# Performance work log

Hardware: AMD Instinct MI355X
Metric: run time of the kernel (lower is better)

The kernel has to match this reference:

```python
import jax, jax.numpy as jnp
import numpy as np

K = 3
KK = K * K
G = 8  # num_heads / offset groups
PAD = K // 2


def conv2d(x, w, b):
    # NCHW conv, stride 1, same padding
    y = jax.lax.conv_general_dilated(
        x, w, window_strides=(1, 1), padding=[(PAD, PAD), (PAD, PAD)],
        dimension_numbers=("NCHW", "OIHW", "NCHW"))
    return y + b[None, :, None, None]


def bilinear_sample(img, py, px):
    # img: [Cg, H, W]; py/px: [KK, H, W] fractional sampling locations
    # zero-padding bilinear (torchvision deform_conv2d semantics)
    Cg, H, W = img.shape
    flat = img.reshape(Cg, H * W)

    y0 = jnp.floor(py)
    x0 = jnp.floor(px)
    wy1 = py - y0
    wx1 = px - x0
    wy0 = 1.0 - wy1
    wx0 = 1.0 - wx1
    y0i = y0.astype(jnp.int32)
    x0i = x0.astype(jnp.int32)

    def gather(iy, ix):
        valid = (iy >= 0) & (iy < H) & (ix >= 0) & (ix < W)
        idx = jnp.clip(iy, 0, H - 1) * W + jnp.clip(ix, 0, W - 1)
        v = jnp.take(flat, idx.reshape(-1), axis=1).reshape(Cg, KK, H, W)
        return v * valid[None].astype(img.dtype)

    return (gather(y0i, x0i) * (wy0 * wx0)[None]
            + gather(y0i, x0i + 1) * (wy0 * wx1)[None]
            + gather(y0i + 1, x0i) * (wy1 * wx0)[None]
            + gather(y0i + 1, x0i + 1) * (wy1 * wx1)[None])


def setup_inputs() -> dict:
    key = jax.random.key(0)
    ks = jax.random.split(key, 8)
    B, C, H, W = 8, 256, 64, 64
    O = 256
    x = jax.random.normal(ks[0], (B, C, H, W), jnp.float32)
    w_off = jax.random.normal(ks[1], (2 * KK * G, C, K, K), jnp.float32) * 0.01
    b_off = jax.random.normal(ks[2], (2 * KK * G,), jnp.float32) * 0.01
    w_attn = jax.random.normal(ks[3], (KK * G, C, K, K), jnp.float32) * 0.01
    b_attn = jax.random.normal(ks[4], (KK * G,), jnp.float32) * 0.01
    w_out = jax.random.normal(ks[5], (O, C, K, K), jnp.float32) * 0.02
    b_out = jax.random.normal(ks[6], (O,), jnp.float32) * 0.01
    return {"x": x, "w_off": w_off, "b_off": b_off,
            "w_attn": w_attn, "b_attn": b_attn,
            "w_out": w_out, "b_out": b_out}


def reference(x, w_off, b_off, w_attn, b_attn, w_out, b_out):
    B, C, H, W = x.shape
    O = w_out.shape[0]
    Cg = C // G

    # learned offsets: [B, G, KK, 2(dy,dx), H, W]
    off = conv2d(x, w_off, b_off).reshape(B, G, KK, 2, H, W)
    # modulation mask with softmax over the KK kernel taps (per head)
    attn = conv2d(x, w_attn, b_attn).reshape(B, G, KK, H, W)
    attn = jax.nn.softmax(attn, axis=2)

    # base sampling grid for each kernel tap (stride=1, dilation=1)
    ki = (jnp.arange(KK) // K).astype(x.dtype)  # kernel row
    kj = (jnp.arange(KK) % K).astype(x.dtype)   # kernel col
    base_y = jnp.arange(H, dtype=x.dtype)[None, :, None] - PAD + ki[:, None, None]  # [KK,H,1]
    base_x = jnp.arange(W, dtype=x.dtype)[None, None, :] - PAD + kj[:, None, None]  # [KK,1,W]
    py = base_y + off[:, :, :, 0]  # [B,G,KK,H,W]
    px = base_x + off[:, :, :, 1]

    xg = x.reshape(B, G, Cg, H, W)
    # vmap bilinear gather over batch and offset groups -> [B,G,Cg,KK,H,W]
    samp = jax.vmap(jax.vmap(bilinear_sample))(xg, py, px)

    # modulated deformable conv: mask-weight the samples, contract with weights
    wt = w_out.reshape(O, G, Cg, KK)
    out = jnp.einsum("bgnkhw,bgkhw,ognk->bohw", samp, attn, wt)
    return out + b_out[None, :, None, None]
```

## Files before the change

### kernel.cpp

```cpp
#include <hip/hip_runtime.h>

#define BN   8
#define CC   256
#define HH   64
#define WW   64
#define GG   8
#define CG   32
#define KKK  9
#define OO   256
#define HW   (HH*WW)
#define NPAD 256
#define NOUT 216

#define XH   68
#define XROW (XH*256)
#define XB   (XH*XH*256)

typedef __attribute__((ext_vector_type(8))) _Float16 half8;
typedef __attribute__((ext_vector_type(4))) float f32x4;

union U4H8 { uint4 u; half8 h; };

#define LGKM0_BARRIER() do { \
    asm volatile("s_waitcnt lgkmcnt(0)" ::: "memory"); \
    __builtin_amdgcn_s_barrier(); \
    __builtin_amdgcn_sched_barrier(0); \
} while (0)

__global__ void repack_w(const float* __restrict__ w_out, _Float16* __restrict__ wt3) {
    int idx = blockIdx.x * 256 + threadIdx.x;
    if (idx >= GG * KKK * CG * OO) return;
    int e    = idx & 7;
    int lane = (idx >> 3) & 63;
    int ot   = (idx >> 9) & 15;
    int s    = idx >> 13;
    int kk = s % 9;
    int g  = s / 9;
    int oc = ot * 16 + (lane & 15);
    int cg = (lane >> 4) * 8 + e;
    wt3[idx] = (_Float16)w_out[oc * 2304 + (g * 32 + cg) * 9 + kk];
}

__global__ void repack_conv(const float* __restrict__ w_off, const float* __restrict__ b_off,
                            const float* __restrict__ w_attn, const float* __restrict__ b_attn,
                            _Float16* __restrict__ wt_conv, float* __restrict__ bias_c) {
    int idx = blockIdx.x * 256 + threadIdx.x;
    if (idx >= 9 * NPAD * 256) return;
    int e    = idx & 7;
    int lane = (idx >> 3) & 63;
    int ot   = (idx >> 9) & 15;
    int gs   = idx >> 13;
    int tap = gs >> 3;
    int ch  = (gs & 7) * 32 + (lane >> 4) * 8 + e;
    int n   = ot * 16 + (lane & 15);
    float v = 0.f;
    if (n < 144)      v = w_off[(n * 256 + ch) * 9 + tap];
    else if (n < 216) v = w_attn[((n - 144) * 256 + ch) * 9 + tap];
    wt_conv[idx] = (_Float16)v;
    if (idx < 224) {
        float bv = 0.f;
        if (idx < 144)      bv = b_off[idx];
        else if (idx < 216) bv = b_attn[idx - 144];
        bias_c[idx] = bv;
    }
}

__global__ __launch_bounds__(256) void repack_x(const float* __restrict__ x,
                                                _Float16* __restrict__ x_h) {
    __shared__ _Float16 T[64][264];
    const int bid = blockIdx.x;
    const int b = bid & 7, h = bid >> 3;
    const int t = threadIdx.x;
    const float* src = x + (((long)(b * 256 + t)) << 12) + h * 64;
    #pragma unroll
    for (int i = 0; i < 16; ++i) {
        float4 f = ((const float4*)src)[i];
        T[i * 4 + 0][t] = (_Float16)f.x;
        T[i * 4 + 1][t] = (_Float16)f.y;
        T[i * 4 + 2][t] = (_Float16)f.z;
        T[i * 4 + 3][t] = (_Float16)f.w;
    }
    __syncthreads();
    _Float16* dst = x_h + ((long)(b * XH + h + 2) * XH + 2) * 256;
    #pragma unroll
    for (int it = 0; it < 8; ++it) {
        int idx = it * 256 + t;
        int px = idx >> 5, ch = idx & 31;
        uint4 v = *(const uint4*)&T[px][ch * 8];
        *(uint4*)(dst + px * 256 + ch * 8) = v;
    }
}

__global__ __launch_bounds__(512, 4) void conv_mfma(
    const _Float16* __restrict__ x_h, const _Float16* __restrict__ wt_conv,
    const float* __restrict__ bias_c, float* __restrict__ conv_buf) {
    __shared__ alignas(16) char smem[36864];
    _Float16 (*Ald)[2][64][40] = (_Float16 (*)[2][64][40])smem;
    float* red = (float*)smem;

    const int bid = blockIdx.x;
    const int b = bid & 7, h = bid >> 3;
    const int t = threadIdx.x;
    const int lane = t & 63;
    const int wv = t >> 6;
    const int group = wv >> 2;
    const int wg = wv & 3;
    const int tl = t & 255;
    const int px = tl >> 2, cq = tl & 3;
    const int gs0 = group * 36;

    f32x4 acc[4][4];
    #pragma unroll
    for (int i = 0; i < 4; ++i)
        #pragma unroll
        for (int j = 0; j < 4; ++j) acc[i][j] = (f32x4){0.f, 0.f, 0.f, 0.f};

    const _Float16* xb = x_h + (long)b * XB + cq * 8;
    const _Float16* wB = wt_conv + (long)(wg * 256 + lane) * 8;

    uint4 aR;
    uint4 bq0, bq1, bq2, bq3;

    {
        int tap = gs0 >> 3, cc = gs0 & 7;
        int y = h + tap / 3 + 1, xc = px + tap % 3 + 1;
        uint4 a0 = *(const uint4*)(xb + ((long)(y * XH + xc)) * 256 + cc * 32);
        *(uint4*)&Ald[group][0][px][cq * 8] = a0;
    }
    {
        int gsn = gs0 + 1;
        int tap = gsn >> 3, cc = gsn & 7;
        int y = h + tap / 3 + 1, xc = px + tap % 3 + 1;
        aR = *(const uint4*)(xb + ((long)(y * XH + xc)) * 256 + cc * 32);
    }
    {
        const _Float16* wsB = wB + (long)gs0 * 8192;
        bq0 = *(const uint4*)(wsB);
        bq1 = *(const uint4*)(wsB + 512);
        bq2 = *(const uint4*)(wsB + 1024);
        bq3 = *(const uint4*)(wsB + 1536);
    }
    LGKM0_BARRIER();

    for (int s = 0; s < 36; ++s) {
        const int gs = gs0 + s;
        if (s < 35) {
            *(uint4*)&Ald[group][(s + 1) & 1][px][cq * 8] = aR;
        }
        if (s < 34) {
            int gsn = gs + 2;
            int tap = gsn >> 3, cc = gsn & 7;
            int y = h + tap / 3 + 1, xc = px + tap % 3 + 1;
            aR = *(const uint4*)(xb + ((long)(y * XH + xc)) * 256 + cc * 32);
        }
        {
            const int k0 = (lane >> 4) * 8;
            U4H8 b0, b1, b2, b3; b0.u = bq0; b1.u = bq1; b2.u = bq2; b3.u = bq3;
            #pragma unroll
            for (int mi = 0; mi < 4; ++mi) {
                half8 a = *(const half8*)&Ald[group][s & 1][mi * 16 + (lane & 15)][k0];
                acc[mi][0] = __builtin_amdgcn_mfma_f32_16x16x32_f16(a, b0.h, acc[mi][0], 0, 0, 0);
                acc[mi][1] = __builtin_amdgcn_mfma_f32_16x16x32_f16(a, b1.h, acc[mi][1], 0, 0, 0);
                acc[mi][2] = __builtin_amdgcn_mfma_f32_16x16x32_f16(a, b2.h, acc[mi][2], 0, 0, 0);
                acc[mi][3] = __builtin_amdgcn_mfma_f32_16x16x32_f16(a, b3.h, acc[mi][3], 0, 0, 0);
            }
        }
        if (s < 35) {
            const _Float16* wsB = wB + (long)(gs + 1) * 8192;
            bq0 = *(const uint4*)(wsB);
            bq1 = *(const uint4*)(wsB + 512);
            bq2 = *(const uint4*)(wsB + 1024);
            bq3 = *(const uint4*)(wsB + 1536);
        }
        LGKM0_BARRIER();
    }

    #pragma unroll
    for (int r = 0; r < 2; ++r) {
        __syncthreads();
        if (group == 1) {
            #pragma unroll
            for (int m2 = 0; m2 < 2; ++m2)
                #pragma unroll
                for (int j = 0; j < 4; ++j)
                    *(f32x4*)&red[tl * 36 + m2 * 16 + j * 4] = acc[r * 2 + m2][j];
        }
        __syncthreads();
        if (group == 0) {
            #pragma unroll
            for (int m2 = 0; m2 < 2; ++m2)
                #pragma unroll
                for (int j = 0; j < 4; ++j) {
                    f32x4 v = *(const f32x4*)&red[tl * 36 + m2 * 16 + j * 4];
                    acc[r * 2 + m2][j] += v;
                }
        }
    }

    if (group == 0) {
        const int colb = (lane >> 4) * 4;
        #pragma unroll
        for (int mi = 0; mi < 4; ++mi) {
            int px0 = mi * 16 + colb;
            #pragma unroll
            for (int j = 0; j < 4; ++j) {
                int oc = wg * 64 + j * 16 + (lane & 15);
                if (oc < NOUT) {
                    float bb = bias_c[oc];
                    float4 v = make_float4(acc[mi][j][0] + bb, acc[mi][j][1] + bb,
                                           acc[mi][j][2] + bb, acc[mi][j][3] + bb);
                    *(float4*)&conv_buf[((long)b * NOUT + oc) * HW + h * WW + px0] = v;
                }
            }
        }
    }
}

__device__ __forceinline__ void calc_coords(int h, int px, int ki, int kj,
    float dy, float dx, int& i00,
    float& u00, float& u01, float& u10, float& u11) {
    float py  = (float)(h - 1 + ki) + dy;
    float pxf = (float)(px - 1 + kj) + dx;
    float y0f = floorf(py), x0f = floorf(pxf);
    float wy1 = py - y0f, wx1 = pxf - x0f;
    float wy0 = 1.f - wy1, wx0 = 1.f - wx1;
    int y0 = min(max((int)y0f, -2), 64);
    int x0 = min(max((int)x0f, -2), 64);
    u00 = wy0 * wx0; u01 = wy0 * wx1;
    u10 = wy1 * wx0; u11 = wy1 * wx1;
    i00 = (y0 + 2) * XH + (x0 + 2);
}

__global__ __launch_bounds__(512, 4) void sample_gemm_mfma(
    const _Float16* __restrict__ x_h, const float* __restrict__ conv_buf,
    const _Float16* __restrict__ wt3,
    const float* __restrict__ b_out, float* __restrict__ out) {
    __shared__ alignas(16) char smem[38912];
    _Float16 (*Ald)[2][64][40] = (_Float16 (*)[2][64][40])smem;
    float* attnL = (float*)(smem + 20480);
    float* red = (float*)smem;

    const int bid = blockIdx.x;
    const int b = bid & 7, h = bid >> 3;
    const int t = threadIdx.x;
    const int lane = t & 63;
    const int wv = t >> 6;
    const int group = wv >> 2;
    const int wg = wv & 3;
    const int tl = t & 255;
    const int px = tl >> 2, cq = tl & 3;
    const int gs0 = group * 36;

    f32x4 acc[4][4];
    #pragma unroll
    for (int i = 0; i < 4; ++i)
        #pragma unroll
        for (int j = 0; j < 4; ++j) acc[i][j] = (f32x4){0.f, 0.f, 0.f, 0.f};

    const float* cbase = conv_buf + (long)b * NOUT * HW + h * WW;
    const _Float16* xbase = x_h + (long)b * XB + cq * 8;
    const _Float16* wB3 = wt3 + (long)(wg * 256 + lane) * 8;

    {
        int ppx = t & 63, g = t >> 6;
        const float* ap = cbase + (long)(144 + g * 9) * HW + ppx;
        float v[9];
        float m = -1e30f;
        #pragma unroll
        for (int k = 0; k < 9; ++k) { v[k] = ap[k * HW]; m = fmaxf(m, v[k]); }
        float ssum = 0.f;
        #pragma unroll
        for (int k = 0; k < 9; ++k) { v[k] = __expf(v[k] - m); ssum += v[k]; }
        float inv = 1.f / ssum;
        #pragma unroll
        for (int k = 0; k < 9; ++k) attnL[(g * 9 + k) * 64 + ppx] = v[k] * inv;
    }
    float dy0 = cbase[(2 * gs0) * HW + px], dx0 = cbase[(2 * gs0 + 1) * HW + px];
    __syncthreads();

    uint4 q00, q01, q10, q11;
    float u00, u01, u10, u11;
    float dyN, dxN;
    uint4 bq0, bq1, bq2, bq3;
    {
        int i00;
        float v00, v01, v10, v11;
        calc_coords(h, px, 0, 0, dy0, dx0, i00, v00, v01, v10, v11);
        const _Float16* xg = xbase + (group * 4) * 32 + (long)i00 * 256;
        uint4 a00 = *(const uint4*)(xg);
        uint4 a01 = *(const uint4*)(xg + 256);
        uint4 a10 = *(const uint4*)(xg + XROW);
        uint4 a11 = *(const uint4*)(xg + XROW + 256);
        float av = attnL[gs0 * 64 + px];
        U4H8 h00, h01, h10, h11;
        h00.u = a00; h01.u = a01; h10.u = a10; h11.u = a11;
        half8 rr = h00.h * (_Float16)v00 + h01.h * (_Float16)v01
                 + h10.h * (_Float16)v10 + h11.h * (_Float16)v11;
        rr = rr * (_Float16)av;
        *(half8*)&Ald[group][0][px][cq * 8] = rr;
    }
    {
        float dy1 = cbase[(2 * (gs0 + 1)) * HW + px];
        float dx1 = cbase[(2 * (gs0 + 1) + 1) * HW + px];
        int i00;
        calc_coords(h, px, 0, 1, dy1, dx1, i00, u00, u01, u10, u11);
        const _Float16* xg = xbase + (group * 4) * 32 + (long)i00 * 256;
        q00 = *(const uint4*)(xg);
        q01 = *(const uint4*)(xg + 256);
        q10 = *(const uint4*)(xg + XROW);
        q11 = *(const uint4*)(xg + XROW + 256);
        dyN = cbase[(2 * (gs0 + 2)) * HW + px];
        dxN = cbase[(2 * (gs0 + 2) + 1) * HW + px];
    }
    {
        const _Float16* wsB = wB3 + (long)gs0 * 8192;
        bq0 = *(const uint4*)(wsB);
        bq1 = *(const uint4*)(wsB + 512);
        bq2 = *(const uint4*)(wsB + 1024);
        bq3 = *(const uint4*)(wsB + 1536);
    }
    LGKM0_BARRIER();

    for (int s = 0; s < 36; ++s) {
        const int gs = gs0 + s;
        if (s < 35) {
            float av = attnL[(gs + 1) * 64 + px];
            U4H8 a00, a01, a10, a11;
            a00.u = q00; a01.u = q01; a10.u = q10; a11.u = q11;
            half8 rr = a00.h * (_Float16)u00 + a01.h * (_Float16)u01
                     + a10.h * (_Float16)u10 + a11.h * (_Float16)u11;
            rr = rr * (_Float16)av;
            *(half8*)&Ald[group][(s + 1) & 1][px][cq * 8] = rr;
        }
        if (s < 34) {
            int sn = s + 2;
            int g = group * 4 + sn / 9, kk = sn % 9;
            int i00;
            calc_coords(h, px, kk / 3, kk % 3, dyN, dxN, i00, u00, u01, u10, u11);
            const _Float16* xg = xbase + g * 32 + (long)i00 * 256;
            q00 = *(const uint4*)(xg);
            q01 = *(const uint4*)(xg + 256);
            q10 = *(const uint4*)(xg + XROW);
            q11 = *(const uint4*)(xg + XROW + 256);
            int s3 = min(s + 3, 35);
            dyN = cbase[(2 * (gs0 + s3)) * HW + px];
            dxN = cbase[(2 * (gs0 + s3) + 1) * HW + px];
        }
        {
            const int k0 = (lane >> 4) * 8;
            U4H8 b0, b1, b2, b3; b0.u = bq0; b1.u = bq1; b2.u = bq2; b3.u = bq3;
            #pragma unroll
            for (int mi = 0; mi < 4; ++mi) {
                half8 a = *(const half8*)&Ald[group][s & 1][mi * 16 + (lane & 15)][k0];
                acc[mi][0] = __builtin_amdgcn_mfma_f32_16x16x32_f16(a, b0.h, acc[mi][0], 0, 0, 0);
                acc[mi][1] = __builtin_amdgcn_mfma_f32_16x16x32_f16(a, b1.h, acc[mi][1], 0, 0, 0);
                acc[mi][2] = __builtin_amdgcn_mfma_f32_16x16x32_f16(a, b2.h, acc[mi][2], 0, 0, 0);
                acc[mi][3] = __builtin_amdgcn_mfma_f32_16x16x32_f16(a, b3.h, acc[mi][3], 0, 0, 0);
            }
        }
        if (s < 35) {
            const _Float16* wsB = wB3 + (long)(gs + 1) * 8192;
            bq0 = *(const uint4*)(wsB);
            bq1 = *(const uint4*)(wsB + 512);
            bq2 = *(const uint4*)(wsB + 1024);
            bq3 = *(const uint4*)(wsB + 1536);
        }
        LGKM0_BARRIER();
    }

    #pragma unroll
    for (int r = 0; r < 2; ++r) {
        __syncthreads();
        if (group == 1) {
            #pragma unroll
            for (int m2 = 0; m2 < 2; ++m2)
                #pragma unroll
                for (int j = 0; j < 4; ++j)
                    *(f32x4*)&red[tl * 36 + m2 * 16 + j * 4] = acc[r * 2 + m2][j];
        }
        __syncthreads();
        if (group == 0) {
            #pragma unroll
            for (int m2 = 0; m2 < 2; ++m2)
                #pragma unroll
                for (int j = 0; j < 4; ++j) {
                    f32x4 v = *(const f32x4*)&red[tl * 36 + m2 * 16 + j * 4];
                    acc[r * 2 + m2][j] += v;
                }
        }
    }

    if (group == 0) {
        const int colb = (lane >> 4) * 4;
        #pragma unroll
        for (int mi = 0; mi < 4; ++mi) {
            int px0 = mi * 16 + colb;
            #pragma unroll
            for (int j = 0; j < 4; ++j) {
                int oc = wg * 64 + j * 16 + (lane & 15);
                float bb = b_out[oc];
                float4 v = make_float4(acc[mi][j][0] + bb, acc[mi][j][1] + bb,
                                       acc[mi][j][2] + bb, acc[mi][j][3] + bb);
                *(float4*)&out[((long)b * OO + oc) * HW + h * WW + px0] = v;
            }
        }
    }
}

extern "C" void kernel_launch(void* const* d_in, const int* in_sizes, int n_in,
                              void* d_out, int out_size, void* d_ws, size_t ws_size,
                              hipStream_t stream) {
    const float* x      = (const float*)d_in[0];
    const float* w_off  = (const float*)d_in[1];
    const float* b_off  = (const float*)d_in[2];
    const float* w_attn = (const float*)d_in[3];
    const float* b_attn = (const float*)d_in[4];
    const float* w_out  = (const float*)d_in[5];
    const float* b_out  = (const float*)d_in[6];
    float* out = (float*)d_out;

    _Float16* x_h     = (_Float16*)d_ws;
    float* conv_buf   = (float*)(x_h + 9469952);
    _Float16* wt3     = (_Float16*)(conv_buf + 7077888);
    _Float16* wt_conv = wt3 + 589824;
    float* bias_c     = (float*)(wt_conv + 589824);

    hipMemsetAsync(x_h, 0, (size_t)9469952 * sizeof(_Float16), stream);

    repack_w<<<dim3((589824 + 255) / 256), dim3(256), 0, stream>>>(w_out, wt3);
    repack_conv<<<dim3((9 * NPAD * 256 + 255) / 256), dim3(256), 0, stream>>>(
        w_off, b_off, w_attn, b_attn, wt_conv, bias_c);
    repack_x<<<dim3(512), dim3(256), 0, stream>>>(x, x_h);

    conv_mfma<<<dim3(512), dim3(512), 0, stream>>>(x_h, wt_conv, bias_c, conv_buf);

    sample_gemm_mfma<<<dim3(512), dim3(512), 0, stream>>>(
        x_h, conv_buf, wt3, b_out, out);
}
```

Before: 215.9 us.

## Double the K-step per pipeline stage to halve barriers in both MFMA kernels

Both the offset/attention conv GEMM and the sampling GEMM now process two 32-wide K slices per loop iteration instead of one. The LDS tile widens from 40 to 72 halves per row, and the register prefetch of A and B operands is doubled. This halves the number of iterations and block-wide barriers and gives more memory parallelism per stage. In exchange it raises register pressure and the sample kernel's shared memory (to 54 KB), which may lower occupancy under launch_bounds(512,4).

New measurement: 330.8 us. 53.3% more time.

```diff
diff --git a/kernel.cpp b/kernel.cpp
--- a/kernel.cpp
+++ b/kernel.cpp
@@ -95,7 +95,7 @@
     const _Float16* __restrict__ x_h, const _Float16* __restrict__ wt_conv,
     const float* __restrict__ bias_c, float* __restrict__ conv_buf) {
     __shared__ alignas(16) char smem[36864];
-    _Float16 (*Ald)[2][64][40] = (_Float16 (*)[2][64][40])smem;
+    _Float16 (*Ald)[2][64][72] = (_Float16 (*)[2][64][72])smem;
     float* red = (float*)smem;
 
     const int bid = blockIdx.x;
@@ -118,44 +118,59 @@
     const _Float16* xb = x_h + (long)b * XB + cq * 8;
     const _Float16* wB = wt_conv + (long)(wg * 256 + lane) * 8;
 
-    uint4 aR;
-    uint4 bq0, bq1, bq2, bq3;
-
-    {
-        int tap = gs0 >> 3, cc = gs0 & 7;
+    uint4 aR0, aR1;
+    uint4 ba0, ba1, ba2, ba3;
+    uint4 bb0, bb1, bb2, bb3;
+
+    {
+        int gs = gs0;
+        int tap = gs >> 3, cb = (gs & 7) * 32;
         int y = h + tap / 3 + 1, xc = px + tap % 3 + 1;
-        uint4 a0 = *(const uint4*)(xb + ((long)(y * XH + xc)) * 256 + cc * 32);
+        const _Float16* p = xb + ((long)(y * XH + xc)) * 256 + cb;
+        uint4 a0 = *(const uint4*)(p);
+        uint4 a1 = *(const uint4*)(p + 32);
         *(uint4*)&Ald[group][0][px][cq * 8] = a0;
-    }
-    {
-        int gsn = gs0 + 1;
-        int tap = gsn >> 3, cc = gsn & 7;
+        *(uint4*)&Ald[group][0][px][32 + cq * 8] = a1;
+    }
+    {
+        int gs = gs0 + 2;
+        int tap = gs >> 3, cb = (gs & 7) * 32;
         int y = h + tap / 3 + 1, xc = px + tap % 3 + 1;
-        aR = *(const uint4*)(xb + ((long)(y * XH + xc)) * 256 + cc * 32);
-    }
-    {
-        const _Float16* wsB = wB + (long)gs0 * 8192;
-        bq0 = *(const uint4*)(wsB);
-        bq1 = *(const uint4*)(wsB + 512);
-        bq2 = *(const uint4*)(wsB + 1024);
-        bq3 = *(const uint4*)(wsB + 1536);
+        const _Float16* p = xb + ((long)(y * XH + xc)) * 256 + cb;
+        aR0 = *(const uint4*)(p);
+        aR1 = *(const uint4*)(p + 32);
+    }
+    {
+        const _Float16* wa = wB + (long)gs0 * 8192;
+        ba0 = *(const uint4*)(wa);
+        ba1 = *(const uint4*)(wa + 512);
+        ba2 = *(const uint4*)(wa + 1024);
+        ba3 = *(const uint4*)(wa + 1536);
+        const _Float16* wb_ = wB + (long)(gs0 + 1) * 8192;
+        bb0 = *(const uint4*)(wb_);
+        bb1 = *(const uint4*)(wb_ + 512);
+        bb2 = *(const uint4*)(wb_ + 1024);
+        bb3 = *(const uint4*)(wb_ + 1536);
     }
     LGKM0_BARRIER();
 
-    for (int s = 0; s < 36; ++s) {
-        const int gs = gs0 + s;
-        if (s < 35) {
-            *(uint4*)&Ald[group][(s + 1) & 1][px][cq * 8] = aR;
-        }
-        if (s < 34) {
-            int gsn = gs + 2;
-            int tap = gsn >> 3, cc = gsn & 7;
+    for (int s = 0; s < 18; ++s) {
+        if (s < 17) {
+            *(uint4*)&Ald[group][(s + 1) & 1][px][cq * 8] = aR0;
+            *(uint4*)&Ald[group][(s + 1) & 1][px][32 + cq * 8] = aR1;
+        }
+        if (s < 16) {
+            int gs = gs0 + 2 * (s + 2);
+            int tap = gs >> 3, cb = (gs & 7) * 32;
             int y = h + tap / 3 + 1, xc = px + tap % 3 + 1;
-            aR = *(const uint4*)(xb + ((long)(y * XH + xc)) * 256 + cc * 32);
+            const _Float16* p = xb + ((long)(y * XH + xc)) * 256 + cb;
+            aR0 = *(const uint4*)(p);
+            aR1 = *(const uint4*)(p + 32);
         }
         {
             const int k0 = (lane >> 4) * 8;
-            U4H8 b0, b1, b2, b3; b0.u = bq0; b1.u = bq1; b2.u = bq2; b3.u = bq3;
+            U4H8 b0, b1, b2, b3;
+            b0.u = ba0; b1.u = ba1; b2.u = ba2; b3.u = ba3;
             #pragma unroll
             for (int mi = 0; mi < 4; ++mi) {
                 half8 a = *(const half8*)&Ald[group][s & 1][mi * 16 + (lane & 15)][k0];
@@ -164,13 +179,28 @@
                 acc[mi][2] = __builtin_amdgcn_mfma_f32_16x16x32_f16(a, b2.h, acc[mi][2], 0, 0, 0);
                 acc[mi][3] = __builtin_amdgcn_mfma_f32_16x16x32_f16(a, b3.h, acc[mi][3], 0, 0, 0);
             }
-        }
-        if (s < 35) {
-            const _Float16* wsB = wB + (long)(gs + 1) * 8192;
-            bq0 = *(const uint4*)(wsB);
-            bq1 = *(const uint4*)(wsB + 512);
-            bq2 = *(const uint4*)(wsB + 1024);
-            bq3 = *(const uint4*)(wsB + 1536);
+            b0.u = bb0; b1.u = bb1; b2.u = bb2; b3.u = bb3;
+            #pragma unroll
+            for (int mi = 0; mi < 4; ++mi) {
+                half8 a = *(const half8*)&Ald[group][s & 1][mi * 16 + (lane & 15)][32 + k0];
+                acc[mi][0] = __builtin_amdgcn_mfma_f32_16x16x32_f16(a, b0.h, acc[mi][0], 0, 0, 0);
+                acc[mi][1] = __builtin_amdgcn_mfma_f32_16x16x32_f16(a, b1.h, acc[mi][1], 0, 0, 0);
+                acc[mi][2] = __builtin_amdgcn_mfma_f32_16x16x32_f16(a, b2.h, acc[mi][2], 0, 0, 0);
+                acc[mi][3] = __builtin_amdgcn_mfma_f32_16x16x32_f16(a, b3.h, acc[mi][3], 0, 0, 0);
+            }
+        }
+        if (s < 17) {
+            int gs = gs0 + 2 * (s + 1);
+            const _Float16* wa = wB + (long)gs * 8192;
+            ba0 = *(const uint4*)(wa);
+            ba1 = *(const uint4*)(wa + 512);
+            ba2 = *(const uint4*)(wa + 1024);
+            ba3 = *(const uint4*)(wa + 1536);
+            const _Float16* wb_ = wB + (long)(gs + 1) * 8192;
+            bb0 = *(const uint4*)(wb_);
+            bb1 = *(const uint4*)(wb_ + 512);
+            bb2 = *(const uint4*)(wb_ + 1024);
+            bb3 = *(const uint4*)(wb_ + 1536);
         }
         LGKM0_BARRIER();
     }
@@ -235,9 +265,9 @@
     const _Float16* __restrict__ x_h, const float* __restrict__ conv_buf,
     const _Float16* __restrict__ wt3,
     const float* __restrict__ b_out, float* __restrict__ out) {
-    __shared__ alignas(16) char smem[38912];
-    _Float16 (*Ald)[2][64][40] = (_Float16 (*)[2][64][40])smem;
-    float* attnL = (float*)(smem + 20480);
+    __shared__ alignas(16) char smem[55296];
+    _Float16 (*Ald)[2][64][72] = (_Float16 (*)[2][64][72])smem;
+    float* attnL = (float*)(smem + 36864);
     float* red = (float*)smem;
 
     const int bid = blockIdx.x;
@@ -275,18 +305,19 @@
         #pragma unroll
         for (int k = 0; k < 9; ++k) attnL[(g * 9 + k) * 64 + ppx] = v[k] * inv;
     }
-    float dy0 = cbase[(2 * gs0) * HW + px], dx0 = cbase[(2 * gs0 + 1) * HW + px];
+    float dyA0 = cbase[(2 * gs0) * HW + px],     dxA0 = cbase[(2 * gs0 + 1) * HW + px];
+    float dyB0 = cbase[(2 * gs0 + 2) * HW + px], dxB0 = cbase[(2 * gs0 + 3) * HW + px];
     __syncthreads();
 
-    uint4 q00, q01, q10, q11;
-    float u00, u01, u10, u11;
-    float dyN, dxN;
-    uint4 bq0, bq1, bq2, bq3;
-    {
-        int i00;
-        float v00, v01, v10, v11;
-        calc_coords(h, px, 0, 0, dy0, dx0, i00, v00, v01, v10, v11);
-        const _Float16* xg = xbase + (group * 4) * 32 + (long)i00 * 256;
+    uint4 qa0, qa1, qa2, qa3;
+    uint4 qb0, qb1, qb2, qb3;
+    float uA00, uA01, uA10, uA11, uB00, uB01, uB10, uB11;
+    float dyA, dxA, dyB, dxB;
+    uint4 ba0, ba1, ba2, ba3, bb0, bb1, bb2, bb3;
+    {
+        int i00; float v00, v01, v10, v11;
+        calc_coords(h, px, 0, 0, dyA0, dxA0, i00, v00, v01, v10, v11);
+        const _Float16* xg = xbase + (gs0 / 9) * 32 + (long)i00 * 256;
         uint4 a00 = *(const uint4*)(xg);
         uint4 a01 = *(const uint4*)(xg + 256);
         uint4 a10 = *(const uint4*)(xg + XROW);
@@ -300,55 +331,98 @@
         *(half8*)&Ald[group][0][px][cq * 8] = rr;
     }
     {
-        float dy1 = cbase[(2 * (gs0 + 1)) * HW + px];
-        float dx1 = cbase[(2 * (gs0 + 1) + 1) * HW + px];
+        int i00; float v00, v01, v10, v11;
+        calc_coords(h, px, 0, 1, dyB0, dxB0, i00, v00, v01, v10, v11);
+        const _Float16* xg = xbase + ((gs0 + 1) / 9) * 32 + (long)i00 * 256;
+        uint4 a00 = *(const uint4*)(xg);
+        uint4 a01 = *(const uint4*)(xg + 256);
+        uint4 a10 = *(const uint4*)(xg + XROW);
+        uint4 a11 = *(const uint4*)(xg + XROW + 256);
+        float av = attnL[(gs0 + 1) * 64 + px];
+        U4H8 h00, h01, h10, h11;
+        h00.u = a00; h01.u = a01; h10.u = a10; h11.u = a11;
+        half8 rr = h00.h * (_Float16)v00 + h01.h * (_Float16)v01
+                 + h10.h * (_Float16)v10 + h11.h * (_Float16)v11;
+        rr = rr * (_Float16)av;
+        *(half8*)&Ald[group][0][px][32 + cq * 8] = rr;
+    }
+    {
+        int tA = gs0 + 2, tB = gs0 + 3;
+        float dya = cbase[(2 * tA) * HW + px], dxa = cbase[(2 * tA + 1) * HW + px];
+        float dyb = cbase[(2 * tB) * HW + px], dxb = cbase[(2 * tB + 1) * HW + px];
         int i00;
-        calc_coords(h, px, 0, 1, dy1, dx1, i00, u00, u01, u10, u11);
-        const _Float16* xg = xbase + (group * 4) * 32 + (long)i00 * 256;
-        q00 = *(const uint4*)(xg);
-        q01 = *(const uint4*)(xg + 256);
-        q10 = *(const uint4*)(xg + XROW);
-        q11 = *(const uint4*)(xg + XROW + 256);
-        dyN = cbase[(2 * (gs0 + 2)) * HW + px];
-        dxN = cbase[(2 * (gs0 + 2) + 1) * HW + px];
-    }
-    {
-        const _Float16* wsB = wB3 + (long)gs0 * 8192;
-        bq0 = *(const uint4*)(wsB);
-        bq1 = *(const uint4*)(wsB + 512);
-        bq2 = *(const uint4*)(wsB + 1024);
-        bq3 = *(const uint4*)(wsB + 1536);
+        calc_coords(h, px, (tA % 9) / 3, (tA % 9) % 3, dya, dxa, i00, uA00, uA01, uA10, uA11);
+        const _Float16* xga = xbase + (tA / 9) * 32 + (long)i00 * 256;
+        qa0 = *(const uint4*)(xga);
+        qa1 = *(const uint4*)(xga + 256);
+        qa2 = *(const uint4*)(xga + XROW);
+        qa3 = *(const uint4*)(xga + XROW + 256);
+        calc_coords(h, px, (tB % 9) / 3, (tB % 9) % 3, dyb, dxb, i00, uB00, uB01, uB10, uB11);
+        const _Float16* xgb = xbase + (tB / 9) * 32 + (long)i00 * 256;
+        qb0 = *(const uint4*)(xgb);
+        qb1 = *(const uint4*)(xgb + 256);
+        qb2 = *(const uint4*)(xgb + XROW);
+        qb3 = *(const uint4*)(xgb + XROW + 256);
+        dyA = cbase[(2 * (gs0 + 4)) * HW + px]; dxA = cbase[(2 * (gs0 + 4) + 1) * HW + px];
+        dyB = cbase[(2 * (gs0 + 5)) * HW + px]; dxB = cbase[(2 * (gs0 + 5) + 1) * HW + px];
+    }
+    {
+        const _Float16* wa = wB3 + (long)gs0 * 8192;
+        ba0 = *(const uint4*)(wa);
+        ba1 = *(const uint4*)(wa + 512);
+        ba2 = *(const uint4*)(wa + 1024);
+        ba3 = *(const uint4*)(wa + 1536);
+        const _Float16* wb_ = wB3 + (long)(gs0 + 1) * 8192;
+        bb0 = *(const uint4*)(wb_);
+        bb1 = *(const uint4*)(wb_ + 512);
+        bb2 = *(const uint4*)(wb_ + 1024);
+        bb3 = *(const uint4*)(wb_ + 1536);
     }
     LGKM0_BARRIER();
 
-    for (int s = 0; s < 36; ++s) {
-        const int gs = gs0 + s;
-        if (s < 35) {
-            float av = attnL[(gs + 1) * 64 + px];
+    for (int s = 0; s < 18; ++s) {
+        if (s < 17) {
+            int tA = gs0 + 2 * (s + 1), tB = tA + 1;
+            float avA = attnL[tA * 64 + px];
+            float avB = attnL[tB * 64 + px];
             U4H8 a00, a01, a10, a11;
-            a00.u = q00; a01.u = q01; a10.u = q10; a11.u = q11;
-            half8 rr = a00.h * (_Float16)u00 + a01.h * (_Float16)u01
-                     + a10.h * (_Float16)u10 + a11.h * (_Float16)u11;
-            rr = rr * (_Float16)av;
-            *(half8*)&Ald[group][(s + 1) & 1][px][cq * 8] = rr;
-        }
-        if (s < 34) {
-            int sn = s + 2;
-            int g = group * 4 + sn / 9, kk = sn % 9;
+            a00.u = qa0; a01.u = qa1; a10.u = qa2; a11.u = qa3;
+            half8 rrA = a00.h * (_Float16)uA00 + a01.h * (_Float16)uA01
+                      + a10.h * (_Float16)uA10 + a11.h * (_Float16)uA11;
+            rrA = rrA * (_Float16)avA;
+            *(half8*)&Ald[group][(s + 1) & 1][px][cq * 8] = rrA;
+            a00.u = qb0; a01.u = qb1; a10.u = qb2; a11.u = qb3;
+            half8 rrB = a00.h * (_Float16)uB00 + a01.h * (_Float16)uB01
+                      + a10.h * (_Float16)uB10 + a11.h * (_Float16)uB11;
+            rrB = rrB * (_Float16)avB;
+            *(half8*)&Ald[group][(s + 1) & 1][px][32 + cq * 8] = rrB;
+        }
+        if (s < 16) {
+            int tA = gs0 + 2 * (s + 2), tB = tA + 1;
             int i00;
-            calc_coords(h, px, kk / 3, kk % 3, dyN, dxN, i00, u00, u01, u10, u11);
-            const _Float16* xg = xbase + g * 32 + (long)i00 * 256;
-            q00 = *(const uint4*)(xg);
-            q01 = *(const uint4*)(xg + 256);
-            q10 = *(const uint4*)(xg + XROW);
-            q11 = *(const uint4*)(xg + XROW + 256);
-            int s3 = min(s + 3, 35);
-            dyN = cbase[(2 * (gs0 + s3)) * HW + px];
-            dxN = cbase[(2 * (gs0 + s3) + 1) * HW + px];
+            calc_coords(h, px, (tA % 9) / 3, (tA % 9) % 3, dyA, dxA, i00,
+                        uA00, uA01, uA10, uA11);
+            const _Float16* xga = xbase + (tA / 9) * 32 + (long)i00 * 256;
+            qa0 = *(const uint4*)(xga);
+            qa1 = *(const uint4*)(xga + 256);
+            qa2 = *(const uint4*)(xga + XROW);
+            qa3 = *(const uint4*)(xga + XROW + 256);
+            calc_coords(h, px, (tB % 9) / 3, (tB % 9) % 3, dyB, dxB, i00,
+                        uB00, uB01, uB10, uB11);
+            const _Float16* xgb = xbase + (tB / 9) * 32 + (long)i00 * 256;
+            qb0 = *(const uint4*)(xgb);
+            qb1 = *(const uint4*)(xgb + 256);
+            qb2 = *(const uint4*)(xgb + XROW);
+            qb3 = *(const uint4*)(xgb + XROW + 256);
+            int s3 = min(s + 3, 17);
+            int t3 = gs0 + 2 * s3;
+            dyA = cbase[(2 * t3) * HW + px];     dxA = cbase[(2 * t3 + 1) * HW + px];
+            dyB = cbase[(2 * t3 + 2) * HW + px]; dxB = cbase[(2 * t3 + 3) * HW + px];
         }
         {
             const int k0 = (lane >> 4) * 8;
-            U4H8 b0, b1, b2, b3; b0.u = bq0; b1.u = bq1; b2.u = bq2; b3.u = bq3;
+            U4H8 b0, b1, b2, b3;
+            b0.u = ba0; b1.u = ba1; b2.u = ba2; b3.u = ba3;
             #pragma unroll
             for (int mi = 0; mi < 4; ++mi) {
                 half8 a = *(const half8*)&Ald[group][s & 1][mi * 16 + (lane & 15)][k0];
@@ -357,13 +431,28 @@
                 acc[mi][2] = __builtin_amdgcn_mfma_f32_16x16x32_f16(a, b2.h, acc[mi][2], 0, 0, 0);
                 acc[mi][3] = __builtin_amdgcn_mfma_f32_16x16x32_f16(a, b3.h, acc[mi][3], 0, 0, 0);
             }
-        }
-        if (s < 35) {
-            const _Float16* wsB = wB3 + (long)(gs + 1) * 8192;
-            bq0 = *(const uint4*)(wsB);
-            bq1 = *(const uint4*)(wsB + 512);
-            bq2 = *(const uint4*)(wsB + 1024);
-            bq3 = *(const uint4*)(wsB + 1536);
+            b0.u = bb0; b1.u = bb1; b2.u = bb2; b3.u = bb3;
+            #pragma unroll
+            for (int mi = 0; mi < 4; ++mi) {
+                half8 a = *(const half8*)&Ald[group][s & 1][mi * 16 + (lane & 15)][32 + k0];
+                acc[mi][0] = __builtin_amdgcn_mfma_f32_16x16x32_f16(a, b0.h, acc[mi][0], 0, 0, 0);
+                acc[mi][1] = __builtin_amdgcn_mfma_f32_16x16x32_f16(a, b1.h, acc[mi][1], 0, 0, 0);
+                acc[mi][2] = __builtin_amdgcn_mfma_f32_16x16x32_f16(a, b2.h, acc[mi][2], 0, 0, 0);
+                acc[mi][3] = __builtin_amdgcn_mfma_f32_16x16x32_f16(a, b3.h, acc[mi][3], 0, 0, 0);
+            }
+        }
+        if (s < 17) {
+            int gs = gs0 + 2 * (s + 1);
+            const _Float16* wa = wB3 + (long)gs * 8192;
+            ba0 = *(const uint4*)(wa);
+            ba1 = *(const uint4*)(wa + 512);
+            ba2 = *(const uint4*)(wa + 1024);
+            ba3 = *(const uint4*)(wa + 1536);
+            const _Float16* wb_ = wB3 + (long)(gs + 1) * 8192;
+            bb0 = *(const uint4*)(wb_);
+            bb1 = *(const uint4*)(wb_ + 512);
+            bb2 = *(const uint4*)(wb_ + 1024);
+            bb3 = *(const uint4*)(wb_ + 1536);
         }
         LGKM0_BARRIER();
     }
```
